# Kernel optimization log

Hardware: AMD Instinct MI355X
Metric: run time of the kernel (lower is better)

The kernel has to match this reference:

```python
import jax, jax.numpy as jnp
import numpy as np

N_NODES = 10000
N_EDGES = 320000
N_GRAPHS = 64
K = 10
IN_C, HID_C, OUT_C = 128, 256, 128


def setup_inputs() -> dict:
    key = jax.random.key(0)
    ks = jax.random.split(key, 10)
    s_in = 1.0 / np.sqrt(IN_C)
    s_hid = 1.0 / np.sqrt(HID_C)
    return {
        "x": jax.random.normal(ks[0], (N_NODES, IN_C), jnp.float32),
        "W0": jax.random.normal(ks[1], (K, IN_C, HID_C), jnp.float32) * s_in,
        "b0": jnp.zeros((HID_C,), jnp.float32),
        "W1": jax.random.normal(ks[2], (K, HID_C, HID_C), jnp.float32) * s_hid,
        "b1": jnp.zeros((HID_C,), jnp.float32),
        "W2": jax.random.normal(ks[3], (K, HID_C, HID_C), jnp.float32) * s_hid,
        "b2": jnp.zeros((HID_C,), jnp.float32),
        "W_out": jax.random.normal(ks[4], (HID_C, OUT_C), jnp.float32) * s_hid,
        "b_out": jnp.zeros((OUT_C,), jnp.float32),
        "edge_index": jax.random.randint(ks[5], (2, N_EDGES), 0, N_NODES, jnp.int64),
        "batch": jnp.sort(jax.random.randint(ks[6], (N_NODES,), 0, N_GRAPHS, jnp.int64)),
    }


def _edge_norm(src, dst, n):
    # Scaled Laplacian L_hat = 2L/lambda_max - I with lambda_max=2 and sym norm
    # => L_hat = -D^{-1/2} A D^{-1/2} (diagonal entries cancel to 0).
    deg = jnp.zeros((n,), jnp.float32).at[src].add(1.0)
    dis = jnp.where(deg > 0, jax.lax.rsqrt(jnp.maximum(deg, 1.0)), 0.0)
    return -dis[src] * dis[dst]


def _propagate(x, src, dst, w, n):
    # message = w * x[src], aggregated by sum at dst
    return jax.ops.segment_sum(w[:, None] * x[src], dst, num_segments=n)


def _cheb_conv(x, src, dst, w, W, b, n):
    # Tx_0 = x; Tx_1 = L_hat x; Tx_k = 2 L_hat Tx_{k-1} - Tx_{k-2}
    K_ = W.shape[0]
    Tx0 = x
    out = Tx0 @ W[0]
    Tx1 = _propagate(Tx0, src, dst, w, n)
    out = out + Tx1 @ W[1]
    for k in range(2, K_):
        Tx2 = 2.0 * _propagate(Tx1, src, dst, w, n) - Tx0
        out = out + Tx2 @ W[k]
        Tx0, Tx1 = Tx1, Tx2
    return out + b


def reference(x, W0, b0, W1, b1, W2, b2, W_out, b_out, edge_index, batch):
    n = x.shape[0]
    src, dst = edge_index[0], edge_index[1]
    w = _edge_norm(src, dst, n)
    # 3 ChebConv layers, each followed by ReLU (norm=None, dropout=0)
    h = jax.nn.relu(_cheb_conv(x, src, dst, w, W0, b0, n))
    h = jax.nn.relu(_cheb_conv(h, src, dst, w, W1, b1, n))
    h = jax.nn.relu(_cheb_conv(h, src, dst, w, W2, b2, n))
    # global_mean_pool over batch ids
    sums = jax.ops.segment_sum(h, batch, num_segments=N_GRAPHS)
    cnts = jax.ops.segment_sum(jnp.ones((n,), h.dtype), batch, num_segments=N_GRAPHS)
    pooled = sums / jnp.maximum(cnts, 1.0)[:, None]
    return pooled @ W_out + b_out
```

## Files before the change

kernel.cpp:

```cpp
#include <hip/hip_runtime.h>
#include <hip/hip_bf16.h>
#include <cstdint>
#include <cstddef>

#define N_NODES 10000
#define N_EDGES 320000
#define N_GRAPHS 64
#define KCHEB 10
#define C_IN 128
#define C_HID 256
#define C_OUTC 128
#define POOL_CHUNK 40

static inline size_t align_up(size_t v, size_t a){ return (v + a - 1) / a * a; }

typedef __attribute__((ext_vector_type(8))) short short8;
typedef __attribute__((ext_vector_type(4))) float f32x4;

__device__ inline float bf2f(unsigned int bits16){
  union{ unsigned int i; float f; } v; v.i = bits16 << 16; return v.f;
}
__device__ inline unsigned short f2bf_bits(float f){
  __hip_bfloat16 h = __float2bfloat16(f);
  return *reinterpret_cast<unsigned short*>(&h);
}


__global__ void k_deg(const int* __restrict__ src, const int* __restrict__ dst,
                      int* __restrict__ deg, int* __restrict__ indeg){
  int e = blockIdx.x*blockDim.x + threadIdx.x;
  if(e < N_EDGES){
    atomicAdd(&deg[src[e]], 1);
    atomicAdd(&indeg[dst[e]], 1);
  }
}

__global__ void k_dis(const int* __restrict__ deg, float* __restrict__ dis){
  int i = blockIdx.x*blockDim.x + threadIdx.x;
  if(i < N_NODES){
    int d = deg[i];
    dis[i] = d > 0 ? rsqrtf((float)d) : 0.f;
  }
}

__global__ void k_edgew(const int* __restrict__ src, const int* __restrict__ dst,
                        const float* __restrict__ dis, float* __restrict__ w){
  int e = blockIdx.x*blockDim.x + threadIdx.x;
  if(e < N_EDGES){
    w[e] = -dis[src[e]] * dis[dst[e]];
  }
}

__global__ __launch_bounds__(1024) void k_scan(const int* __restrict__ cnt,
                                               int* __restrict__ offs,
                                               int* __restrict__ cursor){
  __shared__ int part[1024];
  const int n = N_NODES;
  const int CH = (n + 1023) / 1024;
  int tid = threadIdx.x;
  int base = tid * CH;
  int s = 0;
  for(int i = 0; i < CH; i++){
    int idx = base + i;
    if(idx < n) s += cnt[idx];
  }
  part[tid] = s;
  __syncthreads();
  for(int off = 1; off < 1024; off <<= 1){
    int v = (tid >= off) ? part[tid - off] : 0;
    __syncthreads();
    part[tid] += v;
    __syncthreads();
  }
  int run = (tid == 0) ? 0 : part[tid - 1];
  for(int i = 0; i < CH; i++){
    int idx = base + i;
    if(idx < n){
      offs[idx] = run;
      cursor[idx] = run;
      run += cnt[idx];
    }
  }
  if(tid == 1023) offs[n] = part[1023];
}

__global__ void k_scatter(const int* __restrict__ src, const int* __restrict__ dst,
                          const float* __restrict__ w, int* __restrict__ cursor,
                          int* __restrict__ csr_s, float* __restrict__ csr_w){
  int e = blockIdx.x*blockDim.x + threadIdx.x;
  if(e < N_EDGES){
    int d = dst[e];
    int p = atomicAdd(&cursor[d], 1);
    csr_s[p] = src[e];
    csr_w[p] = w[e];
  }
}

__global__ __launch_bounds__(128) void k_gbounds(const int* __restrict__ batch,
                                                 int* __restrict__ gstart,
                                                 int* __restrict__ gcnt){
  int g = threadIdx.x;
  if(g <= N_GRAPHS){
    int lo = 0, hi = N_NODES;
    while(lo < hi){
      int mid = (lo + hi) >> 1;
      if(batch[mid] < g) lo = mid + 1; else hi = mid;
    }
    gstart[g] = lo;
  }
  __syncthreads();
  if(g < N_GRAPHS) gcnt[g] = gstart[g + 1] - gstart[g];
}


__device__ inline void fma8(float* a, uint4 v, float w){
  a[0] += w * bf2f(v.x & 0xffffu); a[1] += w * bf2f(v.x >> 16);
  a[2] += w * bf2f(v.y & 0xffffu); a[3] += w * bf2f(v.y >> 16);
  a[4] += w * bf2f(v.z & 0xffffu); a[5] += w * bf2f(v.z >> 16);
  a[6] += w * bf2f(v.w & 0xffffu); a[7] += w * bf2f(v.w >> 16);
}

__global__ __launch_bounds__(256) void k_prop256(const __hip_bfloat16* __restrict__ Xb,
                                                 const __hip_bfloat16* __restrict__ Pb,
                                                 __hip_bfloat16* __restrict__ tx,
                                                 const int* __restrict__ csr_s,
                                                 const float* __restrict__ csr_w,
                                                 const int* __restrict__ offs,
                                                 float alpha){
  const int stride = KCHEB * C_HID;
  int hl   = threadIdx.x & 31;
  int b32  = threadIdx.x & 32;
  int node = blockIdx.x * 8 + (threadIdx.x >> 5);
  int j0 = offs[node], j1 = offs[node + 1];
  float a[8] = {};
  const __hip_bfloat16* __restrict__ gbase = Xb + hl * 8;
  int j = j0;
  int sv = 0; float wv = 0.f;
  bool have = (j + 7 < j1);
  if(have){ sv = csr_s[j + (hl & 7)]; wv = csr_w[j + (hl & 7)]; }
  while(have){
    int jn = j + 8;
    bool more = (jn + 7 < j1);
    int sv2 = 0; float wv2 = 0.f;
    if(more){ sv2 = csr_s[jn + (hl & 7)]; wv2 = csr_w[jn + (hl & 7)]; }
    uint4 v[8];
#pragma unroll
    for(int i = 0; i < 8; i++){
      int si = __shfl(sv, b32 + i);
      v[i] = *(const uint4*)(gbase + (size_t)si * stride);
    }
#pragma unroll
    for(int i = 0; i < 8; i++){
      float wi = __shfl(wv, b32 + i);
      fma8(a, v[i], wi);
    }
    sv = sv2; wv = wv2; j = jn; have = more;
  }
  for(; j < j1; j++){
    uint4 v0 = *(const uint4*)(gbase + (size_t)csr_s[j] * stride);
    fma8(a, v0, csr_w[j]);
  }
  float r[8];
#pragma unroll
  for(int i = 0; i < 8; i++) r[i] = alpha * a[i];
  size_t off = (size_t)node * stride + hl * 8;
  if(Pb){
    uint4 pv = *(const uint4*)(Pb + off);
    r[0] -= bf2f(pv.x & 0xffffu); r[1] -= bf2f(pv.x >> 16);
    r[2] -= bf2f(pv.y & 0xffffu); r[3] -= bf2f(pv.y >> 16);
    r[4] -= bf2f(pv.z & 0xffffu); r[5] -= bf2f(pv.z >> 16);
    r[6] -= bf2f(pv.w & 0xffffu); r[7] -= bf2f(pv.w >> 16);
  }
  uint4 ob;
  ob.x = (unsigned)f2bf_bits(r[0]) | ((unsigned)f2bf_bits(r[1]) << 16);
  ob.y = (unsigned)f2bf_bits(r[2]) | ((unsigned)f2bf_bits(r[3]) << 16);
  ob.z = (unsigned)f2bf_bits(r[4]) | ((unsigned)f2bf_bits(r[5]) << 16);
  ob.w = (unsigned)f2bf_bits(r[6]) | ((unsigned)f2bf_bits(r[7]) << 16);
  *(uint4*)(tx + off) = ob;
}

__global__ __launch_bounds__(256) void k_prop128(const __hip_bfloat16* __restrict__ Xb,
                                                 const __hip_bfloat16* __restrict__ Pb,
                                                 __hip_bfloat16* __restrict__ tx,
                                                 const int* __restrict__ csr_s,
                                                 const float* __restrict__ csr_w,
                                                 const int* __restrict__ offs,
                                                 float alpha){
  const int stride = KCHEB * C_IN;
  int hl   = threadIdx.x & 31;
  int b32  = threadIdx.x & 32;
  int node = blockIdx.x * 8 + (threadIdx.x >> 5);
  int j0 = offs[node], j1 = offs[node + 1];
  float a[4] = {};
  const __hip_bfloat16* __restrict__ gbase = Xb + hl * 4;
  int j = j0;
  int sv = 0; float wv = 0.f;
  bool have = (j + 7 < j1);
  if(have){ sv = csr_s[j + (hl & 7)]; wv = csr_w[j + (hl & 7)]; }
  while(have){
    int jn = j + 8;
    bool more = (jn + 7 < j1);
    int sv2 = 0; float wv2 = 0.f;
    if(more){ sv2 = csr_s[jn + (hl & 7)]; wv2 = csr_w[jn + (hl & 7)]; }
    uint2 v[8];
#pragma unroll
    for(int i = 0; i < 8; i++){
      int si = __shfl(sv, b32 + i);
      v[i] = *(const uint2*)(gbase + (size_t)si * stride);
    }
#pragma unroll
    for(int i = 0; i < 8; i++){
      float wi = __shfl(wv, b32 + i);
      a[0] += wi * bf2f(v[i].x & 0xffffu); a[1] += wi * bf2f(v[i].x >> 16);
      a[2] += wi * bf2f(v[i].y & 0xffffu); a[3] += wi * bf2f(v[i].y >> 16);
    }
    sv = sv2; wv = wv2; j = jn; have = more;
  }
  for(; j < j1; j++){
    float w0 = csr_w[j];
    uint2 v0 = *(const uint2*)(gbase + (size_t)csr_s[j] * stride);
    a[0] += w0 * bf2f(v0.x & 0xffffu); a[1] += w0 * bf2f(v0.x >> 16);
    a[2] += w0 * bf2f(v0.y & 0xffffu); a[3] += w0 * bf2f(v0.y >> 16);
  }
  float r0 = alpha * a[0], r1 = alpha * a[1], r2 = alpha * a[2], r3 = alpha * a[3];
  size_t off = (size_t)node * stride + hl * 4;
  if(Pb){
    uint2 pv = *(const uint2*)(Pb + off);
    r0 -= bf2f(pv.x & 0xffffu); r1 -= bf2f(pv.x >> 16);
    r2 -= bf2f(pv.y & 0xffffu); r3 -= bf2f(pv.y >> 16);
  }
  uint2 ob;
  ob.x = (unsigned)f2bf_bits(r0) | ((unsigned)f2bf_bits(r1) << 16);
  ob.y = (unsigned)f2bf_bits(r2) | ((unsigned)f2bf_bits(r3) << 16);
  *(uint2*)(tx + off) = ob;
}

template<int C>
__global__ void k_f2bf(const float* __restrict__ X, __hip_bfloat16* __restrict__ tx,
                       int tx_stride){
  int idx = blockIdx.x * blockDim.x + threadIdx.x;
  const int GPR = C / 4;
  if(idx < N_NODES * GPR){
    int r = idx / GPR;
    int c = (idx - r * GPR) * 4;
    float4 v = *(const float4*)(X + (size_t)r * C + c);
    uint2 ob;
    ob.x = (unsigned)f2bf_bits(v.x) | ((unsigned)f2bf_bits(v.y) << 16);
    ob.y = (unsigned)f2bf_bits(v.z) | ((unsigned)f2bf_bits(v.w) << 16);
    *(uint2*)(tx + (size_t)r * tx_stride + c) = ob;
  }
}

__global__ void k_wt3(const float* __restrict__ W0, __hip_bfloat16* __restrict__ WT0,
                      const float* __restrict__ W1, __hip_bfloat16* __restrict__ WT1,
                      const float* __restrict__ W2, __hip_bfloat16* __restrict__ WT2){
  const int n0 = KCHEB * C_IN  * C_HID;
  const int n1 = KCHEB * C_HID * C_HID;
  int idx = blockIdx.x * blockDim.x + threadIdx.x;
  if(idx < n0){
    int Ktot = KCHEB * C_IN;
    int o = idx / Ktot, kc = idx - o * Ktot;
    WT0[idx] = __float2bfloat16(W0[(size_t)kc * 256 + o]);
  } else if(idx < n0 + n1){
    int i = idx - n0;
    int Ktot = KCHEB * C_HID;
    int o = i / Ktot, kc = i - o * Ktot;
    WT1[i] = __float2bfloat16(W1[(size_t)kc * 256 + o]);
  } else if(idx < n0 + 2 * n1){
    int i = idx - n0 - n1;
    int Ktot = KCHEB * C_HID;
    int o = i / Ktot, kc = i - o * Ktot;
    WT2[i] = __float2bfloat16(W2[(size_t)kc * 256 + o]);
  }
}


__global__ __launch_bounds__(256) void k_gemm_f(const __hip_bfloat16* __restrict__ A,
                                                const __hip_bfloat16* __restrict__ BT,
                                                const float* __restrict__ bias,
                                                float* __restrict__ H,
                                                __hip_bfloat16* __restrict__ tx2,
                                                int M, int Ktot){
  int b = blockIdx.x;
  int xcd = b & 7;
  int l = b >> 3;
  int m = xcd + 8 * (l >> 2);
  int n = l & 3;
  if(m * 64 >= M) return;
  int row0 = m * 64, col0 = n * 64;

  __shared__ short As[2][64 * 64];
  __shared__ short Bs[2][64 * 64];
  int tid = threadIdx.x;
  int lane = tid & 63;
  int wave = tid >> 6;
  int l15 = lane & 15;
  int quad = lane >> 4;
  int wm = (wave & 1) * 32;
  int wn = (wave >> 1) * 32;

  int e0 = tid, e1 = tid + 256;
  int r0 = e0 >> 3, g0 = e0 & 7;
  int r1 = e1 >> 3, g1 = e1 & 7;
  int gr0 = row0 + r0, gr1 = row0 + r1;
  int sa0 = r0 * 64 + ((g0 ^ (r0 & 7)) * 8);
  int sa1 = r1 * 64 + ((g1 ^ (r1 & 7)) * 8);

  f32x4 acc[2][2] = {};
  uint4 av0, av1, bv0, bv1;

  auto load = [&](int k0){
    av0 = (gr0 < M) ? *(const uint4*)(A + (size_t)gr0 * Ktot + k0 + g0 * 8)
                    : make_uint4(0u, 0u, 0u, 0u);
    av1 = (gr1 < M) ? *(const uint4*)(A + (size_t)gr1 * Ktot + k0 + g1 * 8)
                    : make_uint4(0u, 0u, 0u, 0u);
    bv0 = *(const uint4*)(BT + (size_t)(col0 + r0) * Ktot + k0 + g0 * 8);
    bv1 = *(const uint4*)(BT + (size_t)(col0 + r1) * Ktot + k0 + g1 * 8);
  };
  auto stor = [&](int buf){
    *(uint4*)(&As[buf][sa0]) = av0;
    *(uint4*)(&As[buf][sa1]) = av1;
    *(uint4*)(&Bs[buf][sa0]) = bv0;
    *(uint4*)(&Bs[buf][sa1]) = bv1;
  };

  load(0);
  stor(0);
  __syncthreads();
  int nk = Ktot >> 6;
  for(int it = 0; it < nk; it++){
    int cur = it & 1;
    if(it + 1 < nk) load((it + 1) << 6);
#pragma unroll
    for(int kk = 0; kk < 64; kk += 32){
      int g = (kk >> 3) + quad;
      short8 a[2], bb[2];
#pragma unroll
      for(int mi = 0; mi < 2; mi++){
        int r = wm + mi * 16 + l15;
        a[mi] = *(const short8*)(&As[cur][r * 64 + ((g ^ (r & 7)) * 8)]);
      }
#pragma unroll
      for(int ni = 0; ni < 2; ni++){
        int nn = wn + ni * 16 + l15;
        bb[ni] = *(const short8*)(&Bs[cur][nn * 64 + ((g ^ (nn & 7)) * 8)]);
      }
#pragma unroll
      for(int mi = 0; mi < 2; mi++)
#pragma unroll
        for(int ni = 0; ni < 2; ni++)
          acc[mi][ni] = __builtin_amdgcn_mfma_f32_16x16x32_bf16(a[mi], bb[ni], acc[mi][ni], 0, 0, 0);
    }
    if(it + 1 < nk){
      stor(cur ^ 1);
      __syncthreads();
    }
  }

  const int K256 = KCHEB * C_HID;
#pragma unroll
  for(int mi = 0; mi < 2; mi++){
#pragma unroll
    for(int ni = 0; ni < 2; ni++){
      int gcol = col0 + wn + ni * 16 + l15;
      float bv = bias[gcol];
#pragma unroll
      for(int r = 0; r < 4; r++){
        int grow = row0 + wm + mi * 16 + quad * 4 + r;
        if(grow < M){
          float v = fmaxf(acc[mi][ni][r] + bv, 0.f);
          if(tx2) tx2[(size_t)grow * K256 + gcol] = __float2bfloat16(v);
          else    H[(size_t)grow * C_HID + gcol] = v;
        }
      }
    }
  }
}


__global__ __launch_bounds__(256) void k_pool2(const float* __restrict__ h,
                                               const int* __restrict__ batch,
                                               float* __restrict__ gsum){
  int c  = threadIdx.x;
  int n0 = blockIdx.x * POOL_CHUNK;
  int n1 = n0 + POOL_CHUNK;
  if(n1 > N_NODES) n1 = N_NODES;
  if(n0 >= n1) return;
  float acc = 0.f;
  int cur = batch[n0];
  for(int n = n0; n < n1; n++){
    int g = batch[n];
    if(g != cur){
      atomicAdd(&gsum[cur * C_HID + c], acc);
      acc = 0.f;
      cur = g;
    }
    acc += h[(size_t)n * C_HID + c];
  }
  atomicAdd(&gsum[cur * C_HID + c], acc);
}

__global__ __launch_bounds__(128) void k_final(const float* __restrict__ gsum,
                                               const int* __restrict__ gcnt,
                                               const float* __restrict__ Wout,
                                               const float* __restrict__ bout,
                                               float* __restrict__ out){
  int g = blockIdx.x;
  int o = threadIdx.x;
  float inv = 1.f / fmaxf((float)gcnt[g], 1.f);
  float acc = bout[o];
  for(int c = 0; c < C_HID; c++) acc += gsum[g * C_HID + c] * inv * Wout[c * C_OUTC + o];
  out[g * C_OUTC + o] = acc;
}


extern "C" void kernel_launch(void* const* d_in, const int* in_sizes, int n_in,
                              void* d_out, int out_size, void* d_ws, size_t ws_size,
                              hipStream_t stream){
  const float* x    = (const float*)d_in[0];
  const float* W0   = (const float*)d_in[1];
  const float* b0   = (const float*)d_in[2];
  const float* W1   = (const float*)d_in[3];
  const float* b1   = (const float*)d_in[4];
  const float* W2   = (const float*)d_in[5];
  const float* b2   = (const float*)d_in[6];
  const float* Wout = (const float*)d_in[7];
  const float* bout = (const float*)d_in[8];
  const int*   ei   = (const int*)d_in[9];
  const int*   batch= (const int*)d_in[10];
  const int* src = ei;
  const int* dst = ei + N_EDGES;
  float* out = (float*)d_out;

  char* p = (char*)d_ws;
  auto alloc = [&](size_t bytes)->char*{ char* r = p; p += align_up(bytes, 256); return r; };

  int*   deg    = (int*)  alloc(N_NODES * 4);
  int*   indeg  = (int*)  alloc(N_NODES * 4);
  int*   offs   = (int*)  alloc((N_NODES + 1) * 4);
  int*   cursor = (int*)  alloc(N_NODES * 4);
  float* dis    = (float*)alloc(N_NODES * 4);
  float* w_e    = (float*)alloc(N_EDGES * 4);
  int*   csr_s  = (int*)  alloc(N_EDGES * 4);
  float* csr_w  = (float*)alloc(N_EDGES * 4);
  int*   gcnt   = (int*)  alloc(N_GRAPHS * 4);
  int*   gstart = (int*)  alloc((N_GRAPHS + 1) * 4);
  float* gsum   = (float*)alloc(N_GRAPHS * C_HID * 4);

  const size_t txBytes = (size_t)N_NODES * (KCHEB * C_HID) * 2;
  __hip_bfloat16* txP = (__hip_bfloat16*)alloc(txBytes);
  __hip_bfloat16* txQ = (__hip_bfloat16*)alloc(txBytes);
  __hip_bfloat16* WT0 = (__hip_bfloat16*)alloc((size_t)KCHEB * C_IN  * C_HID * 2);
  __hip_bfloat16* WT1 = (__hip_bfloat16*)alloc((size_t)KCHEB * C_HID * C_HID * 2);
  __hip_bfloat16* WT2 = (__hip_bfloat16*)alloc((size_t)KCHEB * C_HID * C_HID * 2);
  float* Hb = (float*)alloc((size_t)N_NODES * C_HID * 4);

  hipMemsetAsync(deg,   0, N_NODES * 4, stream);
  hipMemsetAsync(indeg, 0, N_NODES * 4, stream);
  hipMemsetAsync(gsum,  0, N_GRAPHS * C_HID * 4, stream);

  const int TB = 256;
  int egrid = (N_EDGES + TB - 1) / TB;
  int ngrid = (N_NODES + TB - 1) / TB;

  k_deg<<<egrid, TB, 0, stream>>>(src, dst, deg, indeg);
  k_dis<<<ngrid, TB, 0, stream>>>(deg, dis);
  k_edgew<<<egrid, TB, 0, stream>>>(src, dst, dis, w_e);
  k_scan<<<1, 1024, 0, stream>>>(indeg, offs, cursor);
  k_scatter<<<egrid, TB, 0, stream>>>(src, dst, w_e, cursor, csr_s, csr_w);
  k_gbounds<<<1, 128, 0, stream>>>(batch, gstart, gcnt);

  {
    int ntot = KCHEB * C_IN * C_HID + 2 * KCHEB * C_HID * C_HID;
    k_wt3<<<(ntot + TB - 1) / TB, TB, 0, stream>>>(W0, WT0, W1, WT1, W2, WT2);
  }

  const int K128 = KCHEB * C_IN;
  const int K256 = KCHEB * C_HID;
  const int GEMM_BLOCKS = 640;

  {
    int ng = N_NODES * (C_IN / 4);
    k_f2bf<C_IN><<<(ng + TB - 1) / TB, TB, 0, stream>>>(x, txP, K128);
    for(int k = 1; k < KCHEB; k++){
      const __hip_bfloat16* Xb = txP + (size_t)(k - 1) * C_IN;
      const __hip_bfloat16* Pb = (k >= 2) ? txP + (size_t)(k - 2) * C_IN : nullptr;
      __hip_bfloat16* tx = txP + (size_t)k * C_IN;
      k_prop128<<<N_NODES / 8, 256, 0, stream>>>(Xb, Pb, tx, csr_s, csr_w, offs,
                                                 k == 1 ? 1.f : 2.f);
    }
    k_gemm_f<<<GEMM_BLOCKS, 256, 0, stream>>>(txP, WT0, b0, nullptr, txQ, N_NODES, K128);
  }

  {
    for(int k = 1; k < KCHEB; k++){
      const __hip_bfloat16* Xb = txQ + (size_t)(k - 1) * C_HID;
      const __hip_bfloat16* Pb = (k >= 2) ? txQ + (size_t)(k - 2) * C_HID : nullptr;
      __hip_bfloat16* tx = txQ + (size_t)k * C_HID;
      k_prop256<<<N_NODES / 8, 256, 0, stream>>>(Xb, Pb, tx, csr_s, csr_w, offs,
                                                 k == 1 ? 1.f : 2.f);
    }
    k_gemm_f<<<GEMM_BLOCKS, 256, 0, stream>>>(txQ, WT1, b1, nullptr, txP, N_NODES, K256);
  }

  {
    for(int k = 1; k < KCHEB; k++){
      const __hip_bfloat16* Xb = txP + (size_t)(k - 1) * C_HID;
      const __hip_bfloat16* Pb = (k >= 2) ? txP + (size_t)(k - 2) * C_HID : nullptr;
      __hip_bfloat16* tx = txP + (size_t)k * C_HID;
      k_prop256<<<N_NODES / 8, 256, 0, stream>>>(Xb, Pb, tx, csr_s, csr_w, offs,
                                                 k == 1 ? 1.f : 2.f);
    }
    k_gemm_f<<<GEMM_BLOCKS, 256, 0, stream>>>(txP, WT2, b2, Hb, nullptr, N_NODES, K256);
  }

  k_pool2<<<(N_NODES + POOL_CHUNK - 1) / POOL_CHUNK, 256, 0, stream>>>(Hb, batch, gsum);
  k_final<<<N_GRAPHS, C_OUTC, 0, stream>>>(gsum, gcnt, Wout, bout, out);
}
```

Measured before the change: 685.7 us.

## Stage GEMM tiles with global_load_lds and fold edge-weight kernels into scan/scatter

The dense GEMM now copies its A and B tiles straight from global memory into LDS with global_load_lds, instead of loading into registers and then storing to LDS. The LDS layout changes to a k-group-major arrangement to suit this, and the XOR swizzle is dropped, which may bring back bank conflicts on the MFMA operand reads. Separately, the per-node inverse-sqrt-degree calculation is folded into the scan kernel and the edge weight into the scatter kernel, which removes two launches and an intermediate edge-weight buffer. The A-tile loads no longer check the row bound, so the last partial tile may read past M.

```diff
diff --git a/kernel.cpp b/kernel.cpp
--- a/kernel.cpp
+++ b/kernel.cpp
@@ -25,6 +25,13 @@
   return *reinterpret_cast<unsigned short*>(&h);
 }
 
+__device__ inline void gl_lds16(const void* g, void* l){
+  __builtin_amdgcn_global_load_lds(
+      (const __attribute__((address_space(1))) unsigned int*)g,
+      (__attribute__((address_space(3))) unsigned int*)l,
+      16, 0, 0);
+}
+
 
 __global__ void k_deg(const int* __restrict__ src, const int* __restrict__ dst,
                       int* __restrict__ deg, int* __restrict__ indeg){
@@ -35,25 +42,11 @@
   }
 }
 
-__global__ void k_dis(const int* __restrict__ deg, float* __restrict__ dis){
-  int i = blockIdx.x*blockDim.x + threadIdx.x;
-  if(i < N_NODES){
-    int d = deg[i];
-    dis[i] = d > 0 ? rsqrtf((float)d) : 0.f;
-  }
-}
-
-__global__ void k_edgew(const int* __restrict__ src, const int* __restrict__ dst,
-                        const float* __restrict__ dis, float* __restrict__ w){
-  int e = blockIdx.x*blockDim.x + threadIdx.x;
-  if(e < N_EDGES){
-    w[e] = -dis[src[e]] * dis[dst[e]];
-  }
-}
-
 __global__ __launch_bounds__(1024) void k_scan(const int* __restrict__ cnt,
+                                               const int* __restrict__ deg,
                                                int* __restrict__ offs,
-                                               int* __restrict__ cursor){
+                                               int* __restrict__ cursor,
+                                               float* __restrict__ dis){
   __shared__ int part[1024];
   const int n = N_NODES;
   const int CH = (n + 1023) / 1024;
@@ -79,20 +72,22 @@
       offs[idx] = run;
       cursor[idx] = run;
       run += cnt[idx];
+      int d = deg[idx];
+      dis[idx] = d > 0 ? rsqrtf((float)d) : 0.f;
     }
   }
   if(tid == 1023) offs[n] = part[1023];
 }
 
 __global__ void k_scatter(const int* __restrict__ src, const int* __restrict__ dst,
-                          const float* __restrict__ w, int* __restrict__ cursor,
+                          const float* __restrict__ dis, int* __restrict__ cursor,
                           int* __restrict__ csr_s, float* __restrict__ csr_w){
   int e = blockIdx.x*blockDim.x + threadIdx.x;
   if(e < N_EDGES){
-    int d = dst[e];
+    int s = src[e], d = dst[e];
     int p = atomicAdd(&cursor[d], 1);
-    csr_s[p] = src[e];
-    csr_w[p] = w[e];
+    csr_s[p] = s;
+    csr_w[p] = -dis[s] * dis[d];
   }
 }
 
@@ -289,8 +284,8 @@
   if(m * 64 >= M) return;
   int row0 = m * 64, col0 = n * 64;
 
-  __shared__ short As[2][64 * 64];
-  __shared__ short Bs[2][64 * 64];
+  __shared__ short As[2][8 * 512];
+  __shared__ short Bs[2][8 * 512];
   int tid = threadIdx.x;
   int lane = tid & 63;
   int wave = tid >> 6;
@@ -299,38 +294,24 @@
   int wm = (wave & 1) * 32;
   int wn = (wave >> 1) * 32;
 
-  int e0 = tid, e1 = tid + 256;
-  int r0 = e0 >> 3, g0 = e0 & 7;
-  int r1 = e1 >> 3, g1 = e1 & 7;
-  int gr0 = row0 + r0, gr1 = row0 + r1;
-  int sa0 = r0 * 64 + ((g0 ^ (r0 & 7)) * 8);
-  int sa1 = r1 * 64 + ((g1 ^ (r1 & 7)) * 8);
+  const __hip_bfloat16* pa = A  + (size_t)(row0 + lane) * Ktot;
+  const __hip_bfloat16* pb = BT + (size_t)(col0 + lane) * Ktot;
 
   f32x4 acc[2][2] = {};
-  uint4 av0, av1, bv0, bv1;
-
-  auto load = [&](int k0){
-    av0 = (gr0 < M) ? *(const uint4*)(A + (size_t)gr0 * Ktot + k0 + g0 * 8)
-                    : make_uint4(0u, 0u, 0u, 0u);
-    av1 = (gr1 < M) ? *(const uint4*)(A + (size_t)gr1 * Ktot + k0 + g1 * 8)
-                    : make_uint4(0u, 0u, 0u, 0u);
-    bv0 = *(const uint4*)(BT + (size_t)(col0 + r0) * Ktot + k0 + g0 * 8);
-    bv1 = *(const uint4*)(BT + (size_t)(col0 + r1) * Ktot + k0 + g1 * 8);
+
+  auto stage = [&](int k0, int buf){
+    gl_lds16(pa + k0 + wave * 8,       &As[buf][ wave      * 512]);
+    gl_lds16(pa + k0 + (wave + 4) * 8, &As[buf][(wave + 4) * 512]);
+    gl_lds16(pb + k0 + wave * 8,       &Bs[buf][ wave      * 512]);
+    gl_lds16(pb + k0 + (wave + 4) * 8, &Bs[buf][(wave + 4) * 512]);
   };
-  auto stor = [&](int buf){
-    *(uint4*)(&As[buf][sa0]) = av0;
-    *(uint4*)(&As[buf][sa1]) = av1;
-    *(uint4*)(&Bs[buf][sa0]) = bv0;
-    *(uint4*)(&Bs[buf][sa1]) = bv1;
-  };
-
-  load(0);
-  stor(0);
+
+  stage(0, 0);
   __syncthreads();
   int nk = Ktot >> 6;
   for(int it = 0; it < nk; it++){
     int cur = it & 1;
-    if(it + 1 < nk) load((it + 1) << 6);
+    if(it + 1 < nk) stage((it + 1) << 6, cur ^ 1);
 #pragma unroll
     for(int kk = 0; kk < 64; kk += 32){
       int g = (kk >> 3) + quad;
@@ -338,12 +319,12 @@
 #pragma unroll
       for(int mi = 0; mi < 2; mi++){
         int r = wm + mi * 16 + l15;
-        a[mi] = *(const short8*)(&As[cur][r * 64 + ((g ^ (r & 7)) * 8)]);
+        a[mi] = *(const short8*)(&As[cur][g * 512 + r * 8]);
       }
 #pragma unroll
       for(int ni = 0; ni < 2; ni++){
         int nn = wn + ni * 16 + l15;
-        bb[ni] = *(const short8*)(&Bs[cur][nn * 64 + ((g ^ (nn & 7)) * 8)]);
+        bb[ni] = *(const short8*)(&Bs[cur][g * 512 + nn * 8]);
       }
 #pragma unroll
       for(int mi = 0; mi < 2; mi++)
@@ -351,10 +332,7 @@
         for(int ni = 0; ni < 2; ni++)
           acc[mi][ni] = __builtin_amdgcn_mfma_f32_16x16x32_bf16(a[mi], bb[ni], acc[mi][ni], 0, 0, 0);
     }
-    if(it + 1 < nk){
-      stor(cur ^ 1);
-      __syncthreads();
-    }
+    __syncthreads();
   }
 
   const int K256 = KCHEB * C_HID;
@@ -440,7 +418,6 @@
   int*   offs   = (int*)  alloc((N_NODES + 1) * 4);
   int*   cursor = (int*)  alloc(N_NODES * 4);
   float* dis    = (float*)alloc(N_NODES * 4);
-  float* w_e    = (float*)alloc(N_EDGES * 4);
   int*   csr_s  = (int*)  alloc(N_EDGES * 4);
   float* csr_w  = (float*)alloc(N_EDGES * 4);
   int*   gcnt   = (int*)  alloc(N_GRAPHS * 4);
@@ -461,13 +438,10 @@
 
   const int TB = 256;
   int egrid = (N_EDGES + TB - 1) / TB;
-  int ngrid = (N_NODES + TB - 1) / TB;
 
   k_deg<<<egrid, TB, 0, stream>>>(src, dst, deg, indeg);
-  k_dis<<<ngrid, TB, 0, stream>>>(deg, dis);
-  k_edgew<<<egrid, TB, 0, stream>>>(src, dst, dis, w_e);
-  k_scan<<<1, 1024, 0, stream>>>(indeg, offs, cursor);
-  k_scatter<<<egrid, TB, 0, stream>>>(src, dst, w_e, cursor, csr_s, csr_w);
+  k_scan<<<1, 1024, 0, stream>>>(indeg, deg, offs, cursor, dis);
+  k_scatter<<<egrid, TB, 0, stream>>>(src, dst, dis, cursor, csr_s, csr_w);
   k_gbounds<<<1, 128, 0, stream>>>(batch, gstart, gcnt);
 
   {
```

Result: slower. 758.8 us (+10.7%).
